# Performance work log

Hardware: AMD Instinct MI355X
Metric: run time of the kernel (lower is better)

Reference implementation:

```python
import jax, jax.numpy as jnp
import numpy as np

B, FAN_IN, FAN_OUT, K = 4096, 4096, 4096, 65536


def setup_inputs() -> dict:
    key = jax.random.key(0)
    k1, k2, k3 = jax.random.split(key, 3)
    a = jax.random.normal(k1, (B, FAN_IN), dtype=jnp.float32)
    # hash table H(i, j) -> bucket k in [0, K); replaces the python defaultdict hh
    hash_idx = jax.random.randint(k2, (FAN_OUT, FAN_IN + 1), 0, K)
    d = FAN_OUT * (FAN_IN + 1) / K  # matches d = fan_out * fan_in / K (fan_in already +1)
    W = jax.random.normal(k3, (K,), dtype=jnp.float32) / d
    return {"a": a, "hash_idx": hash_idx, "W": W}


def reference(a, hash_idx, W):
    # append bias column of ones: a_ext [B, fan_in+1]
    ones = jnp.ones((a.shape[0], 1), dtype=a.dtype)
    a_ext = jnp.concatenate([a, ones], axis=1)
    # virtual weight matrix via hash gather: Wv[i, j] = W[H(i, j)]
    Wv = W[hash_idx]  # [fan_out, fan_in+1]
    # out[b, i] = sum_j a_ext[b, j] * W[H(i, j)]
    # identical math to: a_kj[i,b,k] = sum_{j: H(i,j)=k} a_ext[b,j]; zz = a_kj @ W; zz.T
    return jnp.einsum('bj,ij->bi', a_ext, Wv)
```

## Files before the change

kernel.cpp:

```cpp
#include <hip/hip_runtime.h>
#include <hip/hip_bf16.h>
#include <stdint.h>


#define B_DIM   4096
#define FAN_IN  4096
#define FAN_OUT 4096
#define KD      (FAN_IN + 1)
#define KP      4160
#define NKT     65

#define BM 256
#define BN 256
#define BK 64

typedef __attribute__((ext_vector_type(8))) short  short8;
typedef __attribute__((ext_vector_type(4))) float  floatx4;

__device__ __forceinline__ unsigned short f2bf(float f) {
  union { float f; unsigned u; } v; v.f = f;
  unsigned u = v.u;
  u += 0x7fffu + ((u >> 16) & 1u);
  return (unsigned short)(u >> 16);
}

__device__ __forceinline__ void async16(const void* g, void* l) {
  __builtin_amdgcn_global_load_lds(
      (const __attribute__((address_space(1))) void*)g,
      (__attribute__((address_space(3))) void*)l, 16, 0, 0);
}

__global__ __launch_bounds__(256) void build_aext(
    const float* __restrict__ a, unsigned short* __restrict__ Ae) {
  const int row = blockIdx.x;
  const float* ar = a + (size_t)row * FAN_IN;
  unsigned short* er = Ae + (size_t)row * KP;
  for (int j4 = threadIdx.x; j4 < KP / 4; j4 += 256) {
    const int j = j4 * 4;
    float x0, x1, x2, x3;
    if (j + 3 < FAN_IN) {
      const float4 v = *(const float4*)(ar + j);
      x0 = v.x; x1 = v.y; x2 = v.z; x3 = v.w;
    } else {
      x0 = (j + 0 < FAN_IN) ? ar[j + 0] : ((j + 0 == FAN_IN) ? 1.0f : 0.0f);
      x1 = (j + 1 < FAN_IN) ? ar[j + 1] : ((j + 1 == FAN_IN) ? 1.0f : 0.0f);
      x2 = (j + 2 < FAN_IN) ? ar[j + 2] : ((j + 2 == FAN_IN) ? 1.0f : 0.0f);
      x3 = (j + 3 < FAN_IN) ? ar[j + 3] : ((j + 3 == FAN_IN) ? 1.0f : 0.0f);
    }
    ushort4 o;
    o.x = f2bf(x0); o.y = f2bf(x1); o.z = f2bf(x2); o.w = f2bf(x3);
    *(ushort4*)(er + j) = o;
  }
}

__global__ __launch_bounds__(1024) void build_wv(
    const int* __restrict__ hidx, const float* __restrict__ W,
    unsigned short* __restrict__ Wv) {
  extern __shared__ unsigned short wl[];
  const int t = threadIdx.x;

  const float4* Wf = (const float4*)W;
#pragma unroll
  for (int i = 0; i < 16; i++) {
    const int f4 = i * 1024 + t;
    const float4 v = Wf[f4];
    ushort4 o;
    o.x = f2bf(v.x); o.y = f2bf(v.y); o.z = f2bf(v.z); o.w = f2bf(v.w);
    *(ushort4*)&wl[f4 * 4] = o;
  }
  __syncthreads();

  const int r0 = blockIdx.x * 16;
#pragma unroll 4
  for (int r = 0; r < 16; r++) {
    const int* hr = hidx + (size_t)(r0 + r) * KD;
    unsigned short* wr = Wv + (size_t)(r0 + r) * KP;
    const int j = 4 * t;
    ushort4 o;
    o.x = wl[hr[j + 0]];
    o.y = wl[hr[j + 1]];
    o.z = wl[hr[j + 2]];
    o.w = wl[hr[j + 3]];
    *(ushort4*)(wr + j) = o;
    if (t < 64)
      wr[4096 + t] = (t == 0) ? wl[hr[4096]] : (unsigned short)0;
  }
}


#define STAGE_A(BUF, H, KOFF)                                                      \
  do {                                                                             \
    async16(pa + ((H) * 128 + 0)  * KP + (KOFF),                                   \
            smb + ((BUF) << 15) + ((H) << 14) + dA);                               \
    async16(pa + ((H) * 128 + 64) * KP + (KOFF),                                   \
            smb + ((BUF) << 15) + ((H) << 14) + 8192 + dA);                        \
  } while (0)

#define STAGE_B(BUF, H, KOFF)                                                      \
  do {                                                                             \
    async16(pb + ((H) * 128 + 0)  * KP + (KOFF),                                   \
            smb + 65536 + ((BUF) << 15) + ((H) << 14) + dA);                       \
    async16(pb + ((H) * 128 + 64) * KP + (KOFF),                                   \
            smb + 65536 + ((BUF) << 15) + ((H) << 14) + 8192 + dA);                \
  } while (0)

#define PHASE_MID()                                                                \
  do {                                                                             \
    asm volatile("" ::: "memory");                                                 \
    __builtin_amdgcn_s_barrier();                                                  \
    asm volatile("s_waitcnt lgkmcnt(0)" ::: "memory");                             \
    __builtin_amdgcn_sched_barrier(0);                                             \
    __builtin_amdgcn_s_setprio(1);                                                 \
  } while (0)

#define PHASE_END()                                                                \
  do {                                                                             \
    __builtin_amdgcn_s_setprio(0);                                                 \
    asm volatile("" ::: "memory");                                                 \
    __builtin_amdgcn_s_barrier();                                                  \
    asm volatile("" ::: "memory");                                                 \
  } while (0)

#define PHASE_END_TILE()                                                           \
  do {                                                                             \
    __builtin_amdgcn_s_setprio(0);                                                 \
    asm volatile("s_waitcnt vmcnt(4)" ::: "memory");                               \
    __builtin_amdgcn_s_barrier();                                                  \
    asm volatile("" ::: "memory");                                                 \
  } while (0)

#define MFMA2(ACC, AF, BF)                                                         \
  do {                                                                             \
    ACC = __builtin_amdgcn_mfma_f32_16x16x32_bf16((AF)[0], (BF)[0], ACC, 0, 0, 0); \
    ACC = __builtin_amdgcn_mfma_f32_16x16x32_bf16((AF)[1], (BF)[1], ACC, 0, 0, 0); \
  } while (0)

#define KTILE(P, K1, K2)                                                           \
  do {                                                                             \
    short8 af[4][2], bf[4][2];                                                     \
                       \
    _Pragma("unroll")                                                              \
    for (int mi = 0; mi < 4; ++mi) {                                               \
      af[mi][0] = *(const short8*)(smb + ((P) << 15) + arB + mi * 2048 + abase);   \
      af[mi][1] = *(const short8*)(smb + ((P) << 15) + arB + mi * 2048 + (abase ^ 64)); \
    }                                                                              \
    _Pragma("unroll")                                                              \
    for (int ni = 0; ni < 2; ++ni) {                                               \
      bf[ni][0] = *(const short8*)(smb + ((P) << 15) + brB + ni * 2048 + abase);   \
      bf[ni][1] = *(const short8*)(smb + ((P) << 15) + brB + ni * 2048 + (abase ^ 64)); \
    }                                                                              \
    STAGE_A((P) ^ 1, 1, K1);                                                       \
    PHASE_MID();                                                                   \
    _Pragma("unroll")                                                              \
    for (int mi = 0; mi < 4; ++mi)                                                 \
      _Pragma("unroll")                                                            \
      for (int ni = 0; ni < 2; ++ni) MFMA2(acc[mi][ni], af[mi], bf[ni]);           \
    PHASE_END();                                                                   \
               \
    _Pragma("unroll")                                                              \
    for (int ni = 2; ni < 4; ++ni) {                                               \
      bf[ni][0] = *(const short8*)(smb + ((P) << 15) + brB + ni * 2048 + abase);   \
      bf[ni][1] = *(const short8*)(smb + ((P) << 15) + brB + ni * 2048 + (abase ^ 64)); \
    }                                                                              \
    STAGE_B((P) ^ 1, 1, K1);                                                       \
    PHASE_MID();                                                                   \
    _Pragma("unroll")                                                              \
    for (int mi = 0; mi < 4; ++mi)                                                 \
      _Pragma("unroll")                                                            \
      for (int ni = 2; ni < 4; ++ni) MFMA2(acc[mi][ni], af[mi], bf[ni]);           \
    PHASE_END();                                                                   \
               \
            \
    _Pragma("unroll")                                                              \
    for (int mi = 0; mi < 4; ++mi) {                                               \
      af[mi][0] = *(const short8*)(smb + ((P) << 15) + arB + (mi + 4) * 2048 + abase); \
      af[mi][1] = *(const short8*)(smb + ((P) << 15) + arB + (mi + 4) * 2048 + (abase ^ 64)); \
    }                                                                              \
    STAGE_B((P), 0, K2);                                                           \
    PHASE_MID();                                                                   \
    _Pragma("unroll")                                                              \
    for (int mi = 0; mi < 4; ++mi)                                                 \
      _Pragma("unroll")                                                            \
      for (int ni = 0; ni < 2; ++ni) MFMA2(acc[mi + 4][ni], af[mi], bf[ni]);       \
    PHASE_END();                                                                   \
            \
            \
    STAGE_A((P), 0, K2);                                                           \
    PHASE_MID();                                                                   \
    _Pragma("unroll")                                                              \
    for (int mi = 0; mi < 4; ++mi)                                                 \
      _Pragma("unroll")                                                            \
      for (int ni = 2; ni < 4; ++ni) MFMA2(acc[mi + 4][ni], af[mi], bf[ni]);       \
    PHASE_END_TILE();       \
  } while (0)

__global__ __launch_bounds__(512, 2) void gemm_bt8(
    const unsigned short* __restrict__ A, const unsigned short* __restrict__ Bm,
    float* __restrict__ C, int M, int N) {
  extern __shared__ char smb[];
  const int tid = threadIdx.x;
  const int l   = tid & 63;
  const int w   = tid >> 6;
  const int wm  = w >> 2;
  const int wn  = w & 3;
  const int bm  = blockIdx.y * BM;
  const int bn  = blockIdx.x * BN;
  const int q   = l >> 4;
  const int r   = l & 15;

  const int lrow = l >> 3;
  const int lcol = ((l & 7) ^ lrow) * 8;
  const unsigned short* pa = A  + (size_t)(bm + w * 8 + lrow) * KP + lcol;
  const unsigned short* pb = Bm + (size_t)(bn + w * 8 + lrow) * KP + lcol;
  const int dA = w * 1024;

  const int abase = r * 128 + ((q ^ (r & 7)) << 4);
  const int arB   = wm << 14;
  const int brB   = 65536 + ((wn >> 1) << 14) + ((wn & 1) << 13);

  floatx4 acc[8][4] = {};

  STAGE_A(0, 0, 0); STAGE_A(0, 1, 0);
  STAGE_B(0, 0, 0); STAGE_B(0, 1, 0);
  STAGE_B(1, 0, 64); STAGE_A(1, 0, 64);
  asm volatile("s_waitcnt vmcnt(4)" ::: "memory");
  __builtin_amdgcn_s_barrier();
  asm volatile("" ::: "memory");

  int k1 = 64, k2 = 128;
#pragma unroll 1
  for (int tt = 0; tt < 32; ++tt) {
    const int k2c = (k2 > 4096) ? 4096 : k2;
    const int k3c = (k2 + 64 > 4096) ? 4096 : k2 + 64;
    KTILE(0, k1, k2c);
    KTILE(1, k2c, k3c);
    k1 += 128; k2 += 128;
  }

  {
    short8 af[8][2], bf[4][2];
#pragma unroll
    for (int mi = 0; mi < 8; ++mi) {
      af[mi][0] = *(const short8*)(smb + arB + mi * 2048 + abase);
      af[mi][1] = *(const short8*)(smb + arB + mi * 2048 + (abase ^ 64));
    }
#pragma unroll
    for (int ni = 0; ni < 4; ++ni) {
      bf[ni][0] = *(const short8*)(smb + brB + ni * 2048 + abase);
      bf[ni][1] = *(const short8*)(smb + brB + ni * 2048 + (abase ^ 64));
    }
    asm volatile("s_waitcnt lgkmcnt(0)" ::: "memory");
    __builtin_amdgcn_sched_barrier(0);
    __builtin_amdgcn_s_setprio(1);
#pragma unroll
    for (int mi = 0; mi < 8; ++mi)
#pragma unroll
      for (int ni = 0; ni < 4; ++ni) MFMA2(acc[mi][ni], af[mi], bf[ni]);
    __builtin_amdgcn_s_setprio(0);
  }

  asm volatile("s_waitcnt vmcnt(0)" ::: "memory");

  const int r0 = bm + wm * 128;
  const int c0 = bn + wn * 64;
#pragma unroll
  for (int mi = 0; mi < 8; ++mi)
#pragma unroll
    for (int ni = 0; ni < 4; ++ni) {
      const int row0 = r0 + mi * 16 + q * 4;
      const int col  = c0 + ni * 16 + r;
#pragma unroll
      for (int i = 0; i < 4; ++i)
        C[(size_t)(row0 + i) * N + col] = acc[mi][ni][i];
    }
}

extern "C" void kernel_launch(void* const* d_in, const int* in_sizes, int n_in,
                              void* d_out, int out_size, void* d_ws, size_t ws_size,
                              hipStream_t stream) {
  const float* a    = (const float*)d_in[0];
  const int*   hidx = (const int*)d_in[1];
  const float* W    = (const float*)d_in[2];
  float*       out  = (float*)d_out;

  unsigned short* Ae = (unsigned short*)d_ws;
  unsigned short* Wv = Ae + (size_t)B_DIM * KP;

  static bool attr_set = false;
  if (!attr_set) {
    hipFuncSetAttribute((const void*)gemm_bt8,
                        hipFuncAttributeMaxDynamicSharedMemorySize, 131072);
    hipFuncSetAttribute((const void*)build_wv,
                        hipFuncAttributeMaxDynamicSharedMemorySize, 131072);
    attr_set = true;
  }

  build_aext<<<B_DIM, 256, 0, stream>>>(a, Ae);
  build_wv<<<FAN_OUT / 16, 1024, 131072, stream>>>(hidx, W, Wv);
  gemm_bt8<<<dim3(FAN_OUT / BN, B_DIM / BM), 512, 131072, stream>>>(Ae, Wv, out, B_DIM, FAN_OUT);
}
```

Baseline: 285.0 us.

## Prefetch next k-tile's first A/B fragments during last MFMA phase

Moves the LDS reads for the first A and B fragments of the next k-tile into the final phase of the current tile, so they overlap with MFMAs instead of stalling at the start of the next tile. The fragments are held in persistent registers across tiles. The vmcnt wait that guards the next buffer's readiness moves earlier, to the third phase. This adds register pressure under a 2-wave occupancy bound and creates new ordering requirements on LDS readiness.

```diff
diff --git a/kernel.cpp b/kernel.cpp
--- a/kernel.cpp
+++ b/kernel.cpp
@@ -121,10 +121,10 @@
     asm volatile("" ::: "memory");                                                 \
   } while (0)
 
-#define PHASE_END_TILE()                                                           \
+#define PHASE_END_VM2()                                                            \
   do {                                                                             \
     __builtin_amdgcn_s_setprio(0);                                                 \
-    asm volatile("s_waitcnt vmcnt(4)" ::: "memory");                               \
+    asm volatile("s_waitcnt vmcnt(2)" ::: "memory");                               \
     __builtin_amdgcn_s_barrier();                                                  \
     asm volatile("" ::: "memory");                                                 \
   } while (0)
@@ -137,40 +137,31 @@
 
 #define KTILE(P, K1, K2)                                                           \
   do {                                                                             \
-    short8 af[4][2], bf[4][2];                                                     \
-                       \
-    _Pragma("unroll")                                                              \
-    for (int mi = 0; mi < 4; ++mi) {                                               \
-      af[mi][0] = *(const short8*)(smb + ((P) << 15) + arB + mi * 2048 + abase);   \
-      af[mi][1] = *(const short8*)(smb + ((P) << 15) + arB + mi * 2048 + (abase ^ 64)); \
-    }                                                                              \
-    _Pragma("unroll")                                                              \
-    for (int ni = 0; ni < 2; ++ni) {                                               \
-      bf[ni][0] = *(const short8*)(smb + ((P) << 15) + brB + ni * 2048 + abase);   \
-      bf[ni][1] = *(const short8*)(smb + ((P) << 15) + brB + ni * 2048 + (abase ^ 64)); \
-    }                                                                              \
+    short8 af[4][2], bf[2][2];                                                     \
+                        \
     STAGE_A((P) ^ 1, 1, K1);                                                       \
-    PHASE_MID();                                                                   \
+    PHASE_MID();       \
     _Pragma("unroll")                                                              \
     for (int mi = 0; mi < 4; ++mi)                                                 \
       _Pragma("unroll")                                                            \
-      for (int ni = 0; ni < 2; ++ni) MFMA2(acc[mi][ni], af[mi], bf[ni]);           \
+      for (int ni = 0; ni < 2; ++ni) MFMA2(acc[mi][ni], afp[mi], bfp[ni]);         \
     PHASE_END();                                                                   \
-               \
-    _Pragma("unroll")                                                              \
-    for (int ni = 2; ni < 4; ++ni) {                                               \
-      bf[ni][0] = *(const short8*)(smb + ((P) << 15) + brB + ni * 2048 + abase);   \
-      bf[ni][1] = *(const short8*)(smb + ((P) << 15) + brB + ni * 2048 + (abase ^ 64)); \
+                   \
+    _Pragma("unroll")                                                              \
+    for (int ni = 0; ni < 2; ++ni) {                                               \
+      bf[ni][0] = *(const short8*)(smb + ((P) << 15) + brB + (ni + 2) * 2048 + abase); \
+      bf[ni][1] = *(const short8*)(smb + ((P) << 15) + brB + (ni + 2) * 2048 + (abase ^ 64)); \
     }                                                                              \
     STAGE_B((P) ^ 1, 1, K1);                                                       \
     PHASE_MID();                                                                   \
     _Pragma("unroll")                                                              \
     for (int mi = 0; mi < 4; ++mi)                                                 \
       _Pragma("unroll")                                                            \
-      for (int ni = 2; ni < 4; ++ni) MFMA2(acc[mi][ni], af[mi], bf[ni]);           \
+      for (int ni = 0; ni < 2; ++ni) MFMA2(acc[mi][ni + 2], afp[mi], bf[ni]);      \
     PHASE_END();                                                                   \
-               \
-            \
+          \
+          \
+          \
     _Pragma("unroll")                                                              \
     for (int mi = 0; mi < 4; ++mi) {                                               \
       af[mi][0] = *(const short8*)(smb + ((P) << 15) + arB + (mi + 4) * 2048 + abase); \
@@ -181,17 +172,28 @@
     _Pragma("unroll")                                                              \
     for (int mi = 0; mi < 4; ++mi)                                                 \
       _Pragma("unroll")                                                            \
-      for (int ni = 0; ni < 2; ++ni) MFMA2(acc[mi + 4][ni], af[mi], bf[ni]);       \
-    PHASE_END();                                                                   \
-            \
-            \
+      for (int ni = 0; ni < 2; ++ni) MFMA2(acc[mi + 4][ni], af[mi], bfp[ni]);      \
+    PHASE_END_VM2();                                                               \
+         \
+         \
+         \
     STAGE_A((P), 0, K2);                                                           \
     PHASE_MID();                                                                   \
     _Pragma("unroll")                                                              \
+    for (int mi = 0; mi < 4; ++mi) {                                               \
+      afp[mi][0] = *(const short8*)(smb + (((P) ^ 1) << 15) + arB + mi * 2048 + abase); \
+      afp[mi][1] = *(const short8*)(smb + (((P) ^ 1) << 15) + arB + mi * 2048 + (abase ^ 64)); \
+    }                                                                              \
+    _Pragma("unroll")                                                              \
+    for (int ni = 0; ni < 2; ++ni) {                                               \
+      bfp[ni][0] = *(const short8*)(smb + (((P) ^ 1) << 15) + brB + ni * 2048 + abase); \
+      bfp[ni][1] = *(const short8*)(smb + (((P) ^ 1) << 15) + brB + ni * 2048 + (abase ^ 64)); \
+    }                                                                              \
+    _Pragma("unroll")                                                              \
     for (int mi = 0; mi < 4; ++mi)                                                 \
       _Pragma("unroll")                                                            \
-      for (int ni = 2; ni < 4; ++ni) MFMA2(acc[mi + 4][ni], af[mi], bf[ni]);       \
-    PHASE_END_TILE();       \
+      for (int ni = 0; ni < 2; ++ni) MFMA2(acc[mi + 4][ni + 2], af[mi], bf[ni]);   \
+    PHASE_END();            \
   } while (0)
 
 __global__ __launch_bounds__(512, 2) void gemm_bt8(
@@ -219,6 +221,7 @@
   const int brB   = 65536 + ((wn >> 1) << 14) + ((wn & 1) << 13);
 
   floatx4 acc[8][4] = {};
+  short8 afp[4][2], bfp[2][2];
 
   STAGE_A(0, 0, 0); STAGE_A(0, 1, 0);
   STAGE_B(0, 0, 0); STAGE_B(0, 1, 0);
@@ -226,6 +229,16 @@
   asm volatile("s_waitcnt vmcnt(4)" ::: "memory");
   __builtin_amdgcn_s_barrier();
   asm volatile("" ::: "memory");
+#pragma unroll
+  for (int mi = 0; mi < 4; ++mi) {
+    afp[mi][0] = *(const short8*)(smb + arB + mi * 2048 + abase);
+    afp[mi][1] = *(const short8*)(smb + arB + mi * 2048 + (abase ^ 64));
+  }
+#pragma unroll
+  for (int ni = 0; ni < 2; ++ni) {
+    bfp[ni][0] = *(const short8*)(smb + brB + ni * 2048 + abase);
+    bfp[ni][1] = *(const short8*)(smb + brB + ni * 2048 + (abase ^ 64));
+  }
 
   int k1 = 64, k2 = 128;
 #pragma unroll 1
@@ -238,24 +251,29 @@
   }
 
   {
-    short8 af[8][2], bf[4][2];
-#pragma unroll
-    for (int mi = 0; mi < 8; ++mi) {
-      af[mi][0] = *(const short8*)(smb + arB + mi * 2048 + abase);
-      af[mi][1] = *(const short8*)(smb + arB + mi * 2048 + (abase ^ 64));
+    short8 aft[4][2], bft[2][2];
+#pragma unroll
+    for (int mi = 0; mi < 4; ++mi) {
+      aft[mi][0] = *(const short8*)(smb + arB + (mi + 4) * 2048 + abase);
+      aft[mi][1] = *(const short8*)(smb + arB + (mi + 4) * 2048 + (abase ^ 64));
     }
 #pragma unroll
-    for (int ni = 0; ni < 4; ++ni) {
-      bf[ni][0] = *(const short8*)(smb + brB + ni * 2048 + abase);
-      bf[ni][1] = *(const short8*)(smb + brB + ni * 2048 + (abase ^ 64));
+    for (int ni = 0; ni < 2; ++ni) {
+      bft[ni][0] = *(const short8*)(smb + brB + (ni + 2) * 2048 + abase);
+      bft[ni][1] = *(const short8*)(smb + brB + (ni + 2) * 2048 + (abase ^ 64));
     }
     asm volatile("s_waitcnt lgkmcnt(0)" ::: "memory");
     __builtin_amdgcn_sched_barrier(0);
     __builtin_amdgcn_s_setprio(1);
 #pragma unroll
-    for (int mi = 0; mi < 8; ++mi)
-#pragma unroll
-      for (int ni = 0; ni < 4; ++ni) MFMA2(acc[mi][ni], af[mi], bf[ni]);
+    for (int mi = 0; mi < 4; ++mi)
+#pragma unroll
+      for (int ni = 0; ni < 2; ++ni) {
+        MFMA2(acc[mi][ni],          afp[mi], bfp[ni]);
+        MFMA2(acc[mi][ni + 2],      afp[mi], bft[ni]);
+        MFMA2(acc[mi + 4][ni],      aft[mi], bfp[ni]);
+        MFMA2(acc[mi + 4][ni + 2],  aft[mi], bft[ni]);
+      }
     __builtin_amdgcn_s_setprio(0);
   }
 
```

Measured after the change: 286.8 us. Within noise of the previous version (+0.6%).
